# Optimization experiments

Hardware: AMD Instinct MI355X
Metric: run time of the kernel (lower is better)

Reference implementation:

```python
import jax, jax.numpy as jnp
import numpy as np

N = 50000    # nodes
E = 800000   # edges (avg degree 16)
IN = 256     # in_dim
HID = 256    # hidden_dim
OUT = 128    # out_dim


def setup_inputs() -> dict:
    key = jax.random.key(0)
    ks = jax.random.split(key, 9)
    features = jax.random.normal(ks[0], (N, IN), jnp.float32)
    src = jax.random.randint(ks[1], (E,), 0, N, jnp.int32)
    dst = jax.random.randint(ks[2], (E,), 0, N, jnp.int32)
    noise = jax.random.normal(ks[3], (N, OUT), jnp.float32)
    def glorot(k, shape, fan):
        return jax.random.normal(k, shape, jnp.float32) / np.float32(np.sqrt(fan))
    W1 = glorot(ks[4], (IN, HID), IN);  b1 = jnp.zeros((HID,), jnp.float32)
    W2 = glorot(ks[5], (HID, OUT), HID); b2 = jnp.zeros((OUT,), jnp.float32)
    W3 = glorot(ks[6], (HID, OUT), HID); b3 = jnp.zeros((OUT,), jnp.float32)
    fcW = glorot(ks[7], (HID, IN), IN)   # nn.Linear(in_dim, hidden_dim).weight: [HID, IN]
    return dict(features=features, noise=noise, W1=W1, b1=b1, W2=W2, b2=b2,
                W3=W3, b3=b3, fcW=fcW, src=src, dst=dst)


def _gcn(x, W, b, src, dst, out_norm, in_norm):
    """DGL GraphConv norm='both': D_out^{-1/2} A D_in^{-1/2} X W + b."""
    x = x * out_norm[:, None]          # scale src features by out-deg^{-1/2}
    x = x @ W                          # dense transform (order commutes with SpMM)
    agg = jax.ops.segment_sum(x[src], dst, num_segments=N)  # sparse aggregate
    return agg * in_norm[:, None] + b


def reference(features, noise, W1, b1, W2, b2, W3, b3, fcW, src, dst):
    ones = jnp.ones((E,), jnp.float32)
    out_deg = jax.ops.segment_sum(ones, src, num_segments=N)
    in_deg = jax.ops.segment_sum(ones, dst, num_segments=N)
    out_norm = jnp.maximum(out_deg, 1.0) ** -0.5
    in_norm = jnp.maximum(in_deg, 1.0) ** -0.5

    h = jax.nn.relu(_gcn(features, W1, b1, src, dst, out_norm, in_norm))
    mean = jax.nn.relu(_gcn(h, W2, b2, src, dst, out_norm, in_norm))
    log_std = _gcn(h, W3, b3, src, dst, out_norm, in_norm)  # identity activation
    z = mean + noise * jnp.exp(log_std)
    seq_fts = features @ fcW.T
    return z, h, seq_fts
```

## Files before the change

### kernel.cpp

```cpp
#include <hip/hip_runtime.h>
#include <hip/hip_bf16.h>
#include <stdint.h>

#define IN_DIM 256
#define HID_DIM 256
#define OUT_DIM 128

typedef __attribute__((ext_vector_type(8))) short short8;
typedef __attribute__((ext_vector_type(4))) float floatx4;

__device__ __forceinline__ float bf2f(ushort u) {
  union { uint32_t i; float f; } v; v.i = ((uint32_t)u) << 16; return v.f;
}
__device__ __forceinline__ ushort f2bf(float f) {
  union { float f; uint32_t u; } v; v.f = f;
  uint32_t u = v.u;
  uint32_t r = u + 0x7fffu + ((u >> 16) & 1u);
  return (ushort)(r >> 16);
}

__global__ void f2b_kernel(const float* __restrict__ in, ushort* __restrict__ out, int n) {
  int base = (blockIdx.x * 256 + threadIdx.x) * 4;
  if (base < n) {
    float4 v = *(const float4*)(in + base);
    ushort4 o;
    o.x = f2bf(v.x); o.y = f2bf(v.y); o.z = f2bf(v.z); o.w = f2bf(v.w);
    *(ushort4*)(out + base) = o;
  }
}

__global__ void deg_kernel(const int* __restrict__ src, const int* __restrict__ dst,
                           int* __restrict__ out_deg, int* __restrict__ in_deg, int E) {
  int e = blockIdx.x * 256 + threadIdx.x;
  if (e < E) {
    atomicAdd(&out_deg[src[e]], 1);
    atomicAdd(&in_deg[dst[e]], 1);
  }
}

__global__ void norm_kernel(const int* __restrict__ out_deg, const int* __restrict__ in_deg,
                            float* __restrict__ out_norm, float* __restrict__ in_norm, int N) {
  int n = blockIdx.x * 256 + threadIdx.x;
  if (n < N) {
    int od = out_deg[n]; if (od < 1) od = 1;
    int id = in_deg[n];  if (id < 1) id = 1;
    out_norm[n] = rsqrtf((float)od);
    in_norm[n]  = rsqrtf((float)id);
  }
}

__global__ void scan_sums(const int* __restrict__ deg, int* __restrict__ chunk_sum, int n) {
  __shared__ int lds[256];
  int b = blockIdx.x, t = threadIdx.x;
  int base = b * 1024 + t * 4;
  int s = 0;
  if (base + 3 < n) {
    int4 v = *(const int4*)(deg + base);
    s = v.x + v.y + v.z + v.w;
  } else {
    for (int i = 0; i < 4; ++i) if (base + i < n) s += deg[base + i];
  }
  lds[t] = s;
  __syncthreads();
  for (int off = 128; off > 0; off >>= 1) {
    if (t < off) lds[t] += lds[t + off];
    __syncthreads();
  }
  if (t == 0) chunk_sum[b] = lds[0];
}

__global__ void scan_chunks(const int* __restrict__ chunk_sum, int* __restrict__ chunk_off,
                            int nchunks, int* __restrict__ row_ptr) {
  __shared__ int lds[256];
  int t = threadIdx.x;
  int v = (t < nchunks) ? chunk_sum[t] : 0;
  lds[t] = v;
  __syncthreads();
  for (int off = 1; off < 256; off <<= 1) {
    int add = (t >= off) ? lds[t - off] : 0;
    __syncthreads();
    lds[t] += add;
    __syncthreads();
  }
  if (t < nchunks) chunk_off[t] = lds[t] - v;
  if (t == 0) row_ptr[0] = 0;
}

__global__ void scan_final(const int* __restrict__ deg, const int* __restrict__ chunk_off,
                           int* __restrict__ row_ptr, int n) {
  __shared__ int lds[256];
  int b = blockIdx.x, t = threadIdx.x;
  int base = b * 1024 + t * 4;
  int v[4]; int s = 0;
#pragma unroll
  for (int i = 0; i < 4; ++i) { v[i] = (base + i < n) ? deg[base + i] : 0; s += v[i]; }
  lds[t] = s;
  __syncthreads();
  for (int off = 1; off < 256; off <<= 1) {
    int add = (t >= off) ? lds[t - off] : 0;
    __syncthreads();
    lds[t] += add;
    __syncthreads();
  }
  int run = lds[t] - s + chunk_off[b];
#pragma unroll
  for (int i = 0; i < 4; ++i) {
    run += v[i];
    if (base + i < n) row_ptr[base + i + 1] = run;
  }
}

__global__ void fill_kernel(const int* __restrict__ src, const int* __restrict__ dst,
                            const int* __restrict__ row_ptr, int* __restrict__ fill_cnt,
                            int* __restrict__ edge_src, int E) {
  int e = blockIdx.x * 256 + threadIdx.x;
  if (e < E) {
    int d = dst[e];
    int pos = row_ptr[d] + atomicAdd(&fill_cnt[d], 1);
    edge_src[pos] = src[e];
  }
}

__global__ void prep_weights(const float* __restrict__ W1, const float* __restrict__ W2,
                             const float* __restrict__ W3, const float* __restrict__ b2,
                             const float* __restrict__ b3, ushort* __restrict__ W1T,
                             ushort* __restrict__ WcT, float* __restrict__ bcat) {
  int k = blockIdx.x;
  int n = threadIdx.x;
  W1T[n * 256 + k] = f2bf(W1[k * 256 + n]);
  WcT[n * 256 + k] = f2bf((n < 128) ? W2[k * 128 + n] : W3[k * 128 + (n - 128)]);
  if (k == 0) bcat[n] = (n < 128) ? b2[n] : b3[n - 128];
}

__global__ __launch_bounds__(256) void agg_kernel(
    const ushort* __restrict__ x, const int* __restrict__ row_ptr,
    const int* __restrict__ edge_src, const float* __restrict__ out_norm,
    const float* __restrict__ in_norm, ushort* __restrict__ out, int N) {
  int wave = threadIdx.x >> 6, lane = threadIdx.x & 63;
  int n = blockIdx.x * 4 + wave;
  if (n >= N) return;
  int start = row_ptr[n], end = row_ptr[n + 1];
  float acc0 = 0.f, acc1 = 0.f, acc2 = 0.f, acc3 = 0.f;
  for (int base = start; base < end; base += 64) {
    int cnt = end - base; if (cnt > 64) cnt = 64;
    int e = 0; float w = 0.f;
    if (lane < cnt) {
      e = edge_src[base + lane];
      w = out_norm[e];
    }
    for (int i = 0; i < cnt; ++i) {
      int s = __shfl(e, i);
      float wt = __shfl(w, i);
      uint2 v = *(const uint2*)&x[(size_t)s * 256 + lane * 4];
      acc0 += bf2f((ushort)(v.x & 0xffffu)) * wt;
      acc1 += bf2f((ushort)(v.x >> 16)) * wt;
      acc2 += bf2f((ushort)(v.y & 0xffffu)) * wt;
      acc3 += bf2f((ushort)(v.y >> 16)) * wt;
    }
  }
  float inn = in_norm[n];
  uint2 o;
  o.x = ((uint32_t)f2bf(acc1 * inn) << 16) | (uint32_t)f2bf(acc0 * inn);
  o.y = ((uint32_t)f2bf(acc3 * inn) << 16) | (uint32_t)f2bf(acc2 * inn);
  *(uint2*)&out[(size_t)n * 256 + lane * 4] = o;
}

__global__ __launch_bounds__(256) void gemm_kernel(
    const ushort* __restrict__ A, const ushort* __restrict__ BT,
    const float* __restrict__ bias, float* __restrict__ C32,
    ushort* __restrict__ Cbf, int M, int Nout, int relu) {
  __shared__ alignas(16) ushort A_lds[128 * 40];
  __shared__ alignas(16) ushort B_lds[128 * 40];
  int t = threadIdx.x;
  int m0 = blockIdx.x * 128;
  int n0 = blockIdx.y * 128;
  int wave = t >> 6, lane = t & 63;
  int wm = (wave >> 1) * 64, wn = (wave & 1) * 64;
  int l15 = lane & 15, quad = lane >> 4;

  floatx4 acc[4][4];
#pragma unroll
  for (int i = 0; i < 4; ++i)
#pragma unroll
    for (int j = 0; j < 4; ++j) acc[i][j] = (floatx4)(0.f);

  for (int kc = 0; kc < 256; kc += 32) {
#pragma unroll
    for (int r = 0; r < 2; ++r) {
      int idx = t + r * 256;
      int row = idx >> 2;
      int c8 = (idx & 3) << 3;
      int grow = m0 + row; if (grow > M - 1) grow = M - 1;
      uint4 va = *(const uint4*)(A + (size_t)grow * 256 + kc + c8);
      *(uint4*)&A_lds[row * 40 + c8] = va;
      uint4 vb = *(const uint4*)(BT + (size_t)(n0 + row) * 256 + kc + c8);
      *(uint4*)&B_lds[row * 40 + c8] = vb;
    }
    __syncthreads();
    short8 a[4], b[4];
#pragma unroll
    for (int i = 0; i < 4; ++i) {
      a[i] = *(const short8*)&A_lds[(wm + i * 16 + l15) * 40 + quad * 8];
      b[i] = *(const short8*)&B_lds[(wn + i * 16 + l15) * 40 + quad * 8];
    }
#pragma unroll
    for (int i = 0; i < 4; ++i)
#pragma unroll
      for (int j = 0; j < 4; ++j)
        acc[i][j] = __builtin_amdgcn_mfma_f32_16x16x32_bf16(a[i], b[j], acc[i][j], 0, 0, 0);
    __syncthreads();
  }

#pragma unroll
  for (int i = 0; i < 4; ++i) {
#pragma unroll
    for (int j = 0; j < 4; ++j) {
      int col = n0 + wn + j * 16 + l15;
      float bv = bias ? bias[col] : 0.f;
#pragma unroll
      for (int r = 0; r < 4; ++r) {
        int row = m0 + wm + i * 16 + quad * 4 + r;
        if (row < M) {
          float v = acc[i][j][r] + bv;
          if (relu) v = fmaxf(v, 0.f);
          size_t o = (size_t)row * Nout + col;
          if (C32) C32[o] = v;
          if (Cbf) Cbf[o] = f2bf(v);
        }
      }
    }
  }
}

__global__ void z_kernel(const ushort* __restrict__ tmp, const float* __restrict__ noise,
                         float* __restrict__ z, int N) {
  int idx = blockIdx.x * 256 + threadIdx.x;
  if (idx < N * OUT_DIM) {
    int n = idx >> 7, c = idx & 127;
    float m = bf2f(tmp[(size_t)n * 256 + c]);
    float ls = bf2f(tmp[(size_t)n * 256 + 128 + c]);
    float zz = fmaxf(m, 0.f) + noise[idx] * expf(ls);
    z[idx] = zz;
  }
}

extern "C" void kernel_launch(void* const* d_in, const int* in_sizes, int n_in,
                              void* d_out, int out_size, void* d_ws, size_t ws_size,
                              hipStream_t stream) {
  const float* features = (const float*)d_in[0];
  const float* noise    = (const float*)d_in[1];
  const float* W1 = (const float*)d_in[2];
  const float* b1 = (const float*)d_in[3];
  const float* W2 = (const float*)d_in[4];
  const float* b2 = (const float*)d_in[5];
  const float* W3 = (const float*)d_in[6];
  const float* b3 = (const float*)d_in[7];
  const float* fcW = (const float*)d_in[8];
  const int* src = (const int*)d_in[9];
  const int* dst = (const int*)d_in[10];
  const int N = in_sizes[0] / IN_DIM;
  const int E = in_sizes[9];

  float* out = (float*)d_out;
  float* z_out = out;
  float* h_out = out + (size_t)N * OUT_DIM;
  float* s_out = h_out + (size_t)N * HID_DIM;

  char* w = (char*)d_ws;
  auto carve = [&](size_t bytes) {
    char* p = w;
    w += (bytes + 255) & ~(size_t)255;
    return p;
  };
  ushort* feat_bf = (ushort*)carve((size_t)N * 256 * 2);
  ushort* h_bf    = (ushort*)carve((size_t)N * 256 * 2);
  ushort* agg_buf = (ushort*)carve((size_t)N * 256 * 2);
  ushort* tmp_bf  = (ushort*)carve((size_t)N * 256 * 2);
  ushort* W1T  = (ushort*)carve(256 * 256 * 2);
  ushort* WcT  = (ushort*)carve(256 * 256 * 2);
  ushort* fcWb = (ushort*)carve(256 * 256 * 2);
  float*  bcat = (float*)carve(256 * 4);
  int* degs    = (int*)carve((size_t)3 * N * 4);
  int* out_deg = degs;
  int* in_deg  = degs + N;
  int* fill_cnt = degs + 2 * N;
  float* out_norm = (float*)carve((size_t)N * 4);
  float* in_norm  = (float*)carve((size_t)N * 4);
  int* row_ptr  = (int*)carve((size_t)(N + 1) * 4);
  int* edge_src = (int*)carve((size_t)E * 4);
  int* chunk_sum = (int*)carve(256 * 4);
  int* chunk_off = (int*)carve(256 * 4);

  const int nchunks = (N + 1023) / 1024;

  hipMemsetAsync(degs, 0, (size_t)3 * N * 4, stream);
  deg_kernel<<<(E + 255) / 256, 256, 0, stream>>>(src, dst, out_deg, in_deg, E);
  norm_kernel<<<(N + 255) / 256, 256, 0, stream>>>(out_deg, in_deg, out_norm, in_norm, N);
  scan_sums<<<nchunks, 256, 0, stream>>>(in_deg, chunk_sum, N);
  scan_chunks<<<1, 256, 0, stream>>>(chunk_sum, chunk_off, nchunks, row_ptr);
  scan_final<<<nchunks, 256, 0, stream>>>(in_deg, chunk_off, row_ptr, N);
  fill_kernel<<<(E + 255) / 256, 256, 0, stream>>>(src, dst, row_ptr, fill_cnt, edge_src, E);

  f2b_kernel<<<((N * 256 / 4) + 255) / 256, 256, 0, stream>>>(features, feat_bf, N * 256);
  f2b_kernel<<<((256 * 256 / 4) + 255) / 256, 256, 0, stream>>>(fcW, fcWb, 256 * 256);
  prep_weights<<<256, 256, 0, stream>>>(W1, W2, W3, b2, b3, W1T, WcT, bcat);

  dim3 ggrid((N + 127) / 128, 2);
  agg_kernel<<<(N + 3) / 4, 256, 0, stream>>>(feat_bf, row_ptr, edge_src, out_norm, in_norm, agg_buf, N);
  gemm_kernel<<<ggrid, 256, 0, stream>>>(agg_buf, W1T, b1, h_out, h_bf, N, 256, 1);
  agg_kernel<<<(N + 3) / 4, 256, 0, stream>>>(h_bf, row_ptr, edge_src, out_norm, in_norm, agg_buf, N);
  gemm_kernel<<<ggrid, 256, 0, stream>>>(agg_buf, WcT, bcat, (float*)nullptr, tmp_bf, N, 256, 0);
  z_kernel<<<(N * OUT_DIM + 255) / 256, 256, 0, stream>>>(tmp_bf, noise, z_out, N);
  gemm_kernel<<<ggrid, 256, 0, stream>>>(feat_bf, fcWb, (const float*)nullptr, s_out, (ushort*)nullptr, N, 256, 0);
}
```

Baseline: 576.7 us.

## Precompute edge weights, widen aggregation loads, deepen GEMM K-tile, merge fcW prep

The fill kernel now stores each edge's out-degree norm next to its source index, so aggregation no longer does a dependent gather of out_norm. The aggregation kernel splits each wave into two halves that each load 16-byte rows for two edges per iteration, giving four edges in flight, then combines the halves with a cross-half shuffle. The GEMM K-step grows from 32 to 64 with a wider LDS pitch, halving the number of barriers. The fcW bf16 conversion is folded into prep_weights to save a launch. In exchange, agg uses more registers and pays a final reduction, and the GEMM uses more LDS per block, which may lower occupancy.

```diff
diff --git a/kernel.cpp b/kernel.cpp
--- a/kernel.cpp
+++ b/kernel.cpp
@@ -112,65 +112,85 @@
 
 __global__ void fill_kernel(const int* __restrict__ src, const int* __restrict__ dst,
                             const int* __restrict__ row_ptr, int* __restrict__ fill_cnt,
-                            int* __restrict__ edge_src, int E) {
+                            const float* __restrict__ out_norm,
+                            int* __restrict__ edge_src, float* __restrict__ edge_w, int E) {
   int e = blockIdx.x * 256 + threadIdx.x;
   if (e < E) {
     int d = dst[e];
+    int s = src[e];
     int pos = row_ptr[d] + atomicAdd(&fill_cnt[d], 1);
-    edge_src[pos] = src[e];
+    edge_src[pos] = s;
+    edge_w[pos] = out_norm[s];
   }
 }
 
 __global__ void prep_weights(const float* __restrict__ W1, const float* __restrict__ W2,
                              const float* __restrict__ W3, const float* __restrict__ b2,
-                             const float* __restrict__ b3, ushort* __restrict__ W1T,
-                             ushort* __restrict__ WcT, float* __restrict__ bcat) {
+                             const float* __restrict__ b3, const float* __restrict__ fcW,
+                             ushort* __restrict__ W1T, ushort* __restrict__ WcT,
+                             float* __restrict__ bcat, ushort* __restrict__ fcWb) {
   int k = blockIdx.x;
   int n = threadIdx.x;
   W1T[n * 256 + k] = f2bf(W1[k * 256 + n]);
   WcT[n * 256 + k] = f2bf((n < 128) ? W2[k * 128 + n] : W3[k * 128 + (n - 128)]);
+  fcWb[k * 256 + n] = f2bf(fcW[k * 256 + n]);
   if (k == 0) bcat[n] = (n < 128) ? b2[n] : b3[n - 128];
 }
 
 __global__ __launch_bounds__(256) void agg_kernel(
     const ushort* __restrict__ x, const int* __restrict__ row_ptr,
-    const int* __restrict__ edge_src, const float* __restrict__ out_norm,
+    const int* __restrict__ edge_src, const float* __restrict__ edge_w,
     const float* __restrict__ in_norm, ushort* __restrict__ out, int N) {
   int wave = threadIdx.x >> 6, lane = threadIdx.x & 63;
   int n = blockIdx.x * 4 + wave;
   if (n >= N) return;
+  int half = lane >> 5;
+  int hl = lane & 31;
   int start = row_ptr[n], end = row_ptr[n + 1];
-  float acc0 = 0.f, acc1 = 0.f, acc2 = 0.f, acc3 = 0.f;
-  for (int base = start; base < end; base += 64) {
-    int cnt = end - base; if (cnt > 64) cnt = 64;
-    int e = 0; float w = 0.f;
-    if (lane < cnt) {
-      e = edge_src[base + lane];
-      w = out_norm[e];
-    }
-    for (int i = 0; i < cnt; ++i) {
-      int s = __shfl(e, i);
-      float wt = __shfl(w, i);
-      uint2 v = *(const uint2*)&x[(size_t)s * 256 + lane * 4];
-      acc0 += bf2f((ushort)(v.x & 0xffffu)) * wt;
-      acc1 += bf2f((ushort)(v.x >> 16)) * wt;
-      acc2 += bf2f((ushort)(v.y & 0xffffu)) * wt;
-      acc3 += bf2f((ushort)(v.y >> 16)) * wt;
-    }
-  }
-  float inn = in_norm[n];
-  uint2 o;
-  o.x = ((uint32_t)f2bf(acc1 * inn) << 16) | (uint32_t)f2bf(acc0 * inn);
-  o.y = ((uint32_t)f2bf(acc3 * inn) << 16) | (uint32_t)f2bf(acc2 * inn);
-  *(uint2*)&out[(size_t)n * 256 + lane * 4] = o;
+  float acc[8];
+#pragma unroll
+  for (int k = 0; k < 8; ++k) acc[k] = 0.f;
+
+  for (int base = start; base < end; base += 4) {
+    int i0 = base + half;
+    int i1 = base + 2 + half;
+    int s0 = 0, s1 = 0; float w0 = 0.f, w1 = 0.f;
+    if (i0 < end) { s0 = edge_src[i0]; w0 = edge_w[i0]; }
+    if (i1 < end) { s1 = edge_src[i1]; w1 = edge_w[i1]; }
+    uint4 v0 = *(const uint4*)&x[(size_t)s0 * 256 + hl * 8];
+    uint4 v1 = *(const uint4*)&x[(size_t)s1 * 256 + hl * 8];
+    const uint32_t* p0 = (const uint32_t*)&v0;
+    const uint32_t* p1 = (const uint32_t*)&v1;
+#pragma unroll
+    for (int k = 0; k < 4; ++k) {
+      acc[2 * k]     += bf2f((ushort)(p0[k] & 0xffffu)) * w0;
+      acc[2 * k + 1] += bf2f((ushort)(p0[k] >> 16)) * w0;
+      acc[2 * k]     += bf2f((ushort)(p1[k] & 0xffffu)) * w1;
+      acc[2 * k + 1] += bf2f((ushort)(p1[k] >> 16)) * w1;
+    }
+  }
+#pragma unroll
+  for (int k = 0; k < 8; ++k) acc[k] += __shfl_xor(acc[k], 32, 64);
+
+  if (half == 0) {
+    float inn = in_norm[n];
+    uint4 o;
+    uint32_t* po = (uint32_t*)&o;
+#pragma unroll
+    for (int k = 0; k < 4; ++k) {
+      po[k] = ((uint32_t)f2bf(acc[2 * k + 1] * inn) << 16) |
+              (uint32_t)f2bf(acc[2 * k] * inn);
+    }
+    *(uint4*)&out[(size_t)n * 256 + hl * 8] = o;
+  }
 }
 
 __global__ __launch_bounds__(256) void gemm_kernel(
     const ushort* __restrict__ A, const ushort* __restrict__ BT,
     const float* __restrict__ bias, float* __restrict__ C32,
     ushort* __restrict__ Cbf, int M, int Nout, int relu) {
-  __shared__ alignas(16) ushort A_lds[128 * 40];
-  __shared__ alignas(16) ushort B_lds[128 * 40];
+  __shared__ alignas(16) ushort A_lds[128 * 72];
+  __shared__ alignas(16) ushort B_lds[128 * 72];
   int t = threadIdx.x;
   int m0 = blockIdx.x * 128;
   int n0 = blockIdx.y * 128;
@@ -184,30 +204,33 @@
 #pragma unroll
     for (int j = 0; j < 4; ++j) acc[i][j] = (floatx4)(0.f);
 
-  for (int kc = 0; kc < 256; kc += 32) {
-#pragma unroll
-    for (int r = 0; r < 2; ++r) {
+  for (int kc = 0; kc < 256; kc += 64) {
+#pragma unroll
+    for (int r = 0; r < 4; ++r) {
       int idx = t + r * 256;
-      int row = idx >> 2;
-      int c8 = (idx & 3) << 3;
+      int row = idx >> 3;
+      int c8 = (idx & 7) << 3;
       int grow = m0 + row; if (grow > M - 1) grow = M - 1;
       uint4 va = *(const uint4*)(A + (size_t)grow * 256 + kc + c8);
-      *(uint4*)&A_lds[row * 40 + c8] = va;
+      *(uint4*)&A_lds[row * 72 + c8] = va;
       uint4 vb = *(const uint4*)(BT + (size_t)(n0 + row) * 256 + kc + c8);
-      *(uint4*)&B_lds[row * 40 + c8] = vb;
-    }
-    __syncthreads();
-    short8 a[4], b[4];
-#pragma unroll
-    for (int i = 0; i < 4; ++i) {
-      a[i] = *(const short8*)&A_lds[(wm + i * 16 + l15) * 40 + quad * 8];
-      b[i] = *(const short8*)&B_lds[(wn + i * 16 + l15) * 40 + quad * 8];
-    }
-#pragma unroll
-    for (int i = 0; i < 4; ++i)
-#pragma unroll
-      for (int j = 0; j < 4; ++j)
-        acc[i][j] = __builtin_amdgcn_mfma_f32_16x16x32_bf16(a[i], b[j], acc[i][j], 0, 0, 0);
+      *(uint4*)&B_lds[row * 72 + c8] = vb;
+    }
+    __syncthreads();
+#pragma unroll
+    for (int ko = 0; ko < 2; ++ko) {
+      short8 a[4], b[4];
+#pragma unroll
+      for (int i = 0; i < 4; ++i) {
+        a[i] = *(const short8*)&A_lds[(wm + i * 16 + l15) * 72 + ko * 32 + quad * 8];
+        b[i] = *(const short8*)&B_lds[(wn + i * 16 + l15) * 72 + ko * 32 + quad * 8];
+      }
+#pragma unroll
+      for (int i = 0; i < 4; ++i)
+#pragma unroll
+        for (int j = 0; j < 4; ++j)
+          acc[i][j] = __builtin_amdgcn_mfma_f32_16x16x32_bf16(a[i], b[j], acc[i][j], 0, 0, 0);
+    }
     __syncthreads();
   }
 
@@ -288,6 +311,7 @@
   float* in_norm  = (float*)carve((size_t)N * 4);
   int* row_ptr  = (int*)carve((size_t)(N + 1) * 4);
   int* edge_src = (int*)carve((size_t)E * 4);
+  float* edge_w = (float*)carve((size_t)E * 4);
   int* chunk_sum = (int*)carve(256 * 4);
   int* chunk_off = (int*)carve(256 * 4);
 
@@ -299,16 +323,16 @@
   scan_sums<<<nchunks, 256, 0, stream>>>(in_deg, chunk_sum, N);
   scan_chunks<<<1, 256, 0, stream>>>(chunk_sum, chunk_off, nchunks, row_ptr);
   scan_final<<<nchunks, 256, 0, stream>>>(in_deg, chunk_off, row_ptr, N);
-  fill_kernel<<<(E + 255) / 256, 256, 0, stream>>>(src, dst, row_ptr, fill_cnt, edge_src, E);
+  fill_kernel<<<(E + 255) / 256, 256, 0, stream>>>(src, dst, row_ptr, fill_cnt, out_norm,
+                                                   edge_src, edge_w, E);
 
   f2b_kernel<<<((N * 256 / 4) + 255) / 256, 256, 0, stream>>>(features, feat_bf, N * 256);
-  f2b_kernel<<<((256 * 256 / 4) + 255) / 256, 256, 0, stream>>>(fcW, fcWb, 256 * 256);
-  prep_weights<<<256, 256, 0, stream>>>(W1, W2, W3, b2, b3, W1T, WcT, bcat);
+  prep_weights<<<256, 256, 0, stream>>>(W1, W2, W3, b2, b3, fcW, W1T, WcT, bcat, fcWb);
 
   dim3 ggrid((N + 127) / 128, 2);
-  agg_kernel<<<(N + 3) / 4, 256, 0, stream>>>(feat_bf, row_ptr, edge_src, out_norm, in_norm, agg_buf, N);
+  agg_kernel<<<(N + 3) / 4, 256, 0, stream>>>(feat_bf, row_ptr, edge_src, edge_w, in_norm, agg_buf, N);
   gemm_kernel<<<ggrid, 256, 0, stream>>>(agg_buf, W1T, b1, h_out, h_bf, N, 256, 1);
-  agg_kernel<<<(N + 3) / 4, 256, 0, stream>>>(h_bf, row_ptr, edge_src, out_norm, in_norm, agg_buf, N);
+  agg_kernel<<<(N + 3) / 4, 256, 0, stream>>>(h_bf, row_ptr, edge_src, edge_w, in_norm, agg_buf, N);
   gemm_kernel<<<ggrid, 256, 0, stream>>>(agg_buf, WcT, bcat, (float*)nullptr, tmp_bf, N, 256, 0);
   z_kernel<<<(N * OUT_DIM + 255) / 256, 256, 0, stream>>>(tmp_bf, noise, z_out, N);
   gemm_kernel<<<ggrid, 256, 0, stream>>>(feat_bf, fcWb, (const float*)nullptr, s_out, (ushort*)nullptr, N, 256, 0);
```

New measurement: 587.9 us. Within noise of the previous version (+2.0%).
